# Kernel optimization log

Hardware: AMD Instinct MI355X
Metric: run time of the kernel (lower is better)

The kernel has to match this reference:

```python
import jax, jax.numpy as jnp
import numpy as np

DEPTH = 10          # floor(log2(nIn)) with nIn = 1024
N_NODES = 2 ** DEPTH - 1  # 1023
N_IN = 1024
N_OUT = 1024
N_BATCH = 65536


def _unit_rows(key, n, d):
    w = jax.random.normal(key, (n, d), dtype=jnp.float32)
    return w / jnp.linalg.norm(w, axis=-1, keepdims=True)


def setup_inputs() -> dict:
    key = jax.random.key(0)
    kx, kX, kY = jax.random.split(key, 3)
    x = jax.random.normal(kx, (N_BATCH, N_IN), dtype=jnp.float32)
    X = _unit_rows(kX, N_NODES, N_IN)   # hyperspherical-shell init
    Y = _unit_rows(kY, N_NODES, N_OUT)
    return {"x": x, "X": X, "Y": Y}


def reference(x, X, Y):
    # Fast-feedforward binary-tree routing: at each depth, every sample
    # dots with its current node's X row, accumulates lambda * Y row,
    # then branches left/right based on sign(lambda).
    n_batch = x.shape[0]
    n_out = Y.shape[-1]

    def step(carry, _):
        node, y = carry                            # node: [b] int32, y: [b, nOut]
        lam = jnp.einsum('bi,bi->b', x, X[node])   # gather + dot
        y = y + lam[:, None] * Y[node]             # gather + axpy
        node = node * 2 + 1 + (lam > 0).astype(node.dtype)
        return (node, y), None

    init = (jnp.zeros((n_batch,), dtype=jnp.int32),
            jnp.zeros((n_batch, n_out), dtype=x.dtype))
    (_, y), _ = jax.lax.scan(step, init, None, length=DEPTH)
    return y
```

## Files before the change

### kernel.cpp

```cpp
#include <hip/hip_runtime.h>


constexpr int DEPTH = 10;
constexpr int N_IN  = 1024;
constexpr int N_OUT = 1024;

__global__ __launch_bounds__(256) void fff_fwd(
        const float* __restrict__ xg,
        const float* __restrict__ Xg,
        const float* __restrict__ Yg,
        float* __restrict__ outg,
        int n_batch)
{
    const int lane = threadIdx.x & 63;
    const int wave = blockIdx.x * (blockDim.x >> 6) + (threadIdx.x >> 6);
    if (wave >= n_batch) return;

    const float4* xp = reinterpret_cast<const float4*>(xg + (size_t)wave * N_IN) + lane;
    float4 xv[4];
#pragma unroll
    for (int c = 0; c < 4; ++c) xv[c] = xp[c * 64];

    float4 acc[4];
#pragma unroll
    for (int c = 0; c < 4; ++c) acc[c] = make_float4(0.f, 0.f, 0.f, 0.f);

    int node = 0;
#pragma unroll
    for (int d = 0; d < DEPTH; ++d) {
        const float4* Xp = reinterpret_cast<const float4*>(Xg + (size_t)node * N_IN) + lane;
        const float4* Yp = reinterpret_cast<const float4*>(Yg + (size_t)node * N_IN) + lane;
        float4 xr[4], yr[4];
#pragma unroll
        for (int c = 0; c < 4; ++c) xr[c] = Xp[c * 64];
#pragma unroll
        for (int c = 0; c < 4; ++c) yr[c] = Yp[c * 64];

        double p = 0.0;
#pragma unroll
        for (int c = 0; c < 4; ++c) {
            p = fma((double)xv[c].x, (double)xr[c].x, p);
            p = fma((double)xv[c].y, (double)xr[c].y, p);
            p = fma((double)xv[c].z, (double)xr[c].z, p);
            p = fma((double)xv[c].w, (double)xr[c].w, p);
        }
#pragma unroll
        for (int off = 32; off > 0; off >>= 1)
            p += __shfl_xor(p, off, 64);

        const float lam = (float)p;

#pragma unroll
        for (int c = 0; c < 4; ++c) {
            acc[c].x = fmaf(lam, yr[c].x, acc[c].x);
            acc[c].y = fmaf(lam, yr[c].y, acc[c].y);
            acc[c].z = fmaf(lam, yr[c].z, acc[c].z);
            acc[c].w = fmaf(lam, yr[c].w, acc[c].w);
        }

        const int go_right = (p > 0.0) ? 1 : 0;
        node = __builtin_amdgcn_readfirstlane(node * 2 + 1 + go_right);
    }

    float4* op = reinterpret_cast<float4*>(outg + (size_t)wave * N_OUT) + lane;
#pragma unroll
    for (int c = 0; c < 4; ++c) op[c * 64] = acc[c];
}

extern "C" void kernel_launch(void* const* d_in, const int* in_sizes, int n_in,
                              void* d_out, int out_size, void* d_ws, size_t ws_size,
                              hipStream_t stream) {
    const float* x = (const float*)d_in[0];
    const float* X = (const float*)d_in[1];
    const float* Y = (const float*)d_in[2];
    float* out = (float*)d_out;

    const int n_batch = in_sizes[0] / N_IN;
    const int waves_per_block = 4;
    const int blocks = (n_batch + waves_per_block - 1) / waves_per_block;

    fff_fwd<<<blocks, 256, 0, stream>>>(x, X, Y, out, n_batch);
}
```

Before: 602.2 us.

## Speculatively compute both child dot products to break the tree-routing dependency chain

Each level now loads the X rows of both children and computes their partial dot products before the branch decision is known. The next level then only has to pick one, do the wave reduction and load Y. This hides gather latency behind the reduction and FMA work, and the partial sums are split into four accumulators to shorten the FP64 chain. The cost is roughly twice the X-row traffic and FP64 work, plus higher register pressure.

```diff
diff --git a/kernel.cpp b/kernel.cpp
--- a/kernel.cpp
+++ b/kernel.cpp
@@ -4,6 +4,45 @@
 constexpr int DEPTH = 10;
 constexpr int N_IN  = 1024;
 constexpr int N_OUT = 1024;
+
+__device__ __forceinline__ void load_row(float4 (&dst)[4],
+                                         const float* __restrict__ base,
+                                         int row, int lane)
+{
+    const float4* p = reinterpret_cast<const float4*>(base + (size_t)row * N_IN) + lane;
+#pragma unroll
+    for (int c = 0; c < 4; ++c) dst[c] = p[c * 64];
+}
+
+__device__ __forceinline__ double dot16(const float4 (&a)[4], const float4 (&b)[4])
+{
+    double p0 = 0.0, p1 = 0.0, p2 = 0.0, p3 = 0.0;
+    p0 = fma((double)a[0].x, (double)b[0].x, p0);
+    p0 = fma((double)a[0].y, (double)b[0].y, p0);
+    p0 = fma((double)a[0].z, (double)b[0].z, p0);
+    p0 = fma((double)a[0].w, (double)b[0].w, p0);
+    p1 = fma((double)a[1].x, (double)b[1].x, p1);
+    p1 = fma((double)a[1].y, (double)b[1].y, p1);
+    p1 = fma((double)a[1].z, (double)b[1].z, p1);
+    p1 = fma((double)a[1].w, (double)b[1].w, p1);
+    p2 = fma((double)a[2].x, (double)b[2].x, p2);
+    p2 = fma((double)a[2].y, (double)b[2].y, p2);
+    p2 = fma((double)a[2].z, (double)b[2].z, p2);
+    p2 = fma((double)a[2].w, (double)b[2].w, p2);
+    p3 = fma((double)a[3].x, (double)b[3].x, p3);
+    p3 = fma((double)a[3].y, (double)b[3].y, p3);
+    p3 = fma((double)a[3].z, (double)b[3].z, p3);
+    p3 = fma((double)a[3].w, (double)b[3].w, p3);
+    return (p0 + p1) + (p2 + p3);
+}
+
+__device__ __forceinline__ double wave_sum64(double p)
+{
+#pragma unroll
+    for (int off = 32; off > 0; off >>= 1)
+        p += __shfl_xor(p, off, 64);
+    return p;
+}
 
 __global__ __launch_bounds__(256) void fff_fwd(
         const float* __restrict__ xg,
@@ -25,41 +64,57 @@
 #pragma unroll
     for (int c = 0; c < 4; ++c) acc[c] = make_float4(0.f, 0.f, 0.f, 0.f);
 
-    int node = 0;
+    float4 cur[4], xl[4], xr[4], yv[4];
+    load_row(cur, Xg, 0, lane);
+    load_row(xl,  Xg, 1, lane);
+    load_row(xr,  Xg, 2, lane);
+    load_row(yv,  Yg, 0, lane);
+
+    double p = dot16(xv, cur);
+    p = wave_sum64(p);
+    int   s   = (p > 0.0) ? 1 : 0;
+    float lam = (float)p;
 #pragma unroll
-    for (int d = 0; d < DEPTH; ++d) {
-        const float4* Xp = reinterpret_cast<const float4*>(Xg + (size_t)node * N_IN) + lane;
-        const float4* Yp = reinterpret_cast<const float4*>(Yg + (size_t)node * N_IN) + lane;
-        float4 xr[4], yr[4];
+    for (int c = 0; c < 4; ++c) {
+        acc[c].x = fmaf(lam, yv[c].x, acc[c].x);
+        acc[c].y = fmaf(lam, yv[c].y, acc[c].y);
+        acc[c].z = fmaf(lam, yv[c].z, acc[c].z);
+        acc[c].w = fmaf(lam, yv[c].w, acc[c].w);
+    }
+
+    double pl = dot16(xv, xl);
+    double pr = dot16(xv, xr);
+
+    int node = __builtin_amdgcn_readfirstlane(1 + s);
+
 #pragma unroll
-        for (int c = 0; c < 4; ++c) xr[c] = Xp[c * 64];
-#pragma unroll
-        for (int c = 0; c < 4; ++c) yr[c] = Yp[c * 64];
+    for (int d = 1; d < DEPTH; ++d) {
+        if (d < DEPTH - 1) {
+            load_row(xl, Xg, 2 * node + 1, lane);
+            load_row(xr, Xg, 2 * node + 2, lane);
+        }
+        load_row(yv, Yg, node, lane);
 
-        double p = 0.0;
-#pragma unroll
-        for (int c = 0; c < 4; ++c) {
-            p = fma((double)xv[c].x, (double)xr[c].x, p);
-            p = fma((double)xv[c].y, (double)xr[c].y, p);
-            p = fma((double)xv[c].z, (double)xr[c].z, p);
-            p = fma((double)xv[c].w, (double)xr[c].w, p);
+        p = s ? pr : pl;
+        p = wave_sum64(p);
+        const int snew = (p > 0.0) ? 1 : 0;
+        lam = (float)p;
+
+        if (d < DEPTH - 1) {
+            pl = dot16(xv, xl);
+            pr = dot16(xv, xr);
         }
-#pragma unroll
-        for (int off = 32; off > 0; off >>= 1)
-            p += __shfl_xor(p, off, 64);
-
-        const float lam = (float)p;
 
 #pragma unroll
         for (int c = 0; c < 4; ++c) {
-            acc[c].x = fmaf(lam, yr[c].x, acc[c].x);
-            acc[c].y = fmaf(lam, yr[c].y, acc[c].y);
-            acc[c].z = fmaf(lam, yr[c].z, acc[c].z);
-            acc[c].w = fmaf(lam, yr[c].w, acc[c].w);
+            acc[c].x = fmaf(lam, yv[c].x, acc[c].x);
+            acc[c].y = fmaf(lam, yv[c].y, acc[c].y);
+            acc[c].z = fmaf(lam, yv[c].z, acc[c].z);
+            acc[c].w = fmaf(lam, yv[c].w, acc[c].w);
         }
 
-        const int go_right = (p > 0.0) ? 1 : 0;
-        node = __builtin_amdgcn_readfirstlane(node * 2 + 1 + go_right);
+        s = snew;
+        node = __builtin_amdgcn_readfirstlane(2 * node + 1 + snew);
     }
 
     float4* op = reinterpret_cast<float4*>(outg + (size_t)wave * N_OUT) + lane;
```

After: 685.4 us. 13.8% more time.

## Stage top four tree levels of X and Y in LDS per block

Applied to the files above, without the earlier changes.

Each 1024-thread block copies the first 15 nodes of X and Y (120 KB) into shared memory, then serves the first four tree depths from LDS instead of global memory. The block size grows from 256 to 1024 threads, and the double-precision dot product is split into four independent accumulators to shorten the FMA dependency chain. The per-block LDS fill adds startup cost and the large LDS footprint limits occupancy to about one block per CU. The four-accumulator summation can also change rounding slightly near the sign decision.

```diff
diff --git a/kernel.cpp b/kernel.cpp
--- a/kernel.cpp
+++ b/kernel.cpp
@@ -1,19 +1,76 @@
 #include <hip/hip_runtime.h>
 
 
-constexpr int DEPTH = 10;
-constexpr int N_IN  = 1024;
-constexpr int N_OUT = 1024;
+constexpr int DEPTH     = 10;
+constexpr int N_IN      = 1024;
+constexpr int N_OUT     = 1024;
+constexpr int LDS_DEPTHS = 4;
+constexpr int LDS_NODES  = 15;
+constexpr int THREADS    = 1024;
 
-__global__ __launch_bounds__(256) void fff_fwd(
+__device__ __forceinline__ void load_row4(float4 (&dst)[4], const float* __restrict__ row, int lane)
+{
+    const float4* p = reinterpret_cast<const float4*>(row) + lane;
+#pragma unroll
+    for (int c = 0; c < 4; ++c) dst[c] = p[c * 64];
+}
+
+__device__ __forceinline__ double dot16(const float4 (&a)[4], const float4 (&b)[4])
+{
+    double p0 = 0.0, p1 = 0.0, p2 = 0.0, p3 = 0.0;
+    p0 = fma((double)a[0].x, (double)b[0].x, p0);
+    p0 = fma((double)a[0].y, (double)b[0].y, p0);
+    p0 = fma((double)a[0].z, (double)b[0].z, p0);
+    p0 = fma((double)a[0].w, (double)b[0].w, p0);
+    p1 = fma((double)a[1].x, (double)b[1].x, p1);
+    p1 = fma((double)a[1].y, (double)b[1].y, p1);
+    p1 = fma((double)a[1].z, (double)b[1].z, p1);
+    p1 = fma((double)a[1].w, (double)b[1].w, p1);
+    p2 = fma((double)a[2].x, (double)b[2].x, p2);
+    p2 = fma((double)a[2].y, (double)b[2].y, p2);
+    p2 = fma((double)a[2].z, (double)b[2].z, p2);
+    p2 = fma((double)a[2].w, (double)b[2].w, p2);
+    p3 = fma((double)a[3].x, (double)b[3].x, p3);
+    p3 = fma((double)a[3].y, (double)b[3].y, p3);
+    p3 = fma((double)a[3].z, (double)b[3].z, p3);
+    p3 = fma((double)a[3].w, (double)b[3].w, p3);
+    return (p0 + p1) + (p2 + p3);
+}
+
+__device__ __forceinline__ double wave_sum64(double p)
+{
+#pragma unroll
+    for (int off = 32; off > 0; off >>= 1)
+        p += __shfl_xor(p, off, 64);
+    return p;
+}
+
+__global__ __launch_bounds__(THREADS) void fff_fwd(
         const float* __restrict__ xg,
         const float* __restrict__ Xg,
         const float* __restrict__ Yg,
         float* __restrict__ outg,
         int n_batch)
 {
+    extern __shared__ float lds[];
+    float* sX = lds;
+    float* sY = lds + LDS_NODES * N_IN;
+
+    {
+        const float4* gx4 = reinterpret_cast<const float4*>(Xg);
+        const float4* gy4 = reinterpret_cast<const float4*>(Yg);
+        float4* sx4 = reinterpret_cast<float4*>(sX);
+        float4* sy4 = reinterpret_cast<float4*>(sY);
+        const int n4 = LDS_NODES * N_IN / 4;
+        for (int i = threadIdx.x; i < n4; i += THREADS) {
+            sx4[i] = gx4[i];
+            sy4[i] = gy4[i];
+        }
+    }
+    __syncthreads();
+
     const int lane = threadIdx.x & 63;
-    const int wave = blockIdx.x * (blockDim.x >> 6) + (threadIdx.x >> 6);
+    const int wave = blockIdx.x * (THREADS >> 6) + (threadIdx.x >> 6);
     if (wave >= n_batch) return;
 
     const float4* xp = reinterpret_cast<const float4*>(xg + (size_t)wave * N_IN) + lane;
@@ -28,26 +85,17 @@
     int node = 0;
 #pragma unroll
     for (int d = 0; d < DEPTH; ++d) {
-        const float4* Xp = reinterpret_cast<const float4*>(Xg + (size_t)node * N_IN) + lane;
-        const float4* Yp = reinterpret_cast<const float4*>(Yg + (size_t)node * N_IN) + lane;
         float4 xr[4], yr[4];
-#pragma unroll
-        for (int c = 0; c < 4; ++c) xr[c] = Xp[c * 64];
-#pragma unroll
-        for (int c = 0; c < 4; ++c) yr[c] = Yp[c * 64];
+        if (d < LDS_DEPTHS) {
+            load_row4(xr, sX + node * N_IN, lane);
+            load_row4(yr, sY + node * N_IN, lane);
+        } else {
+            load_row4(xr, Xg + (size_t)node * N_IN, lane);
+            load_row4(yr, Yg + (size_t)node * N_IN, lane);
+        }
 
-        double p = 0.0;
-#pragma unroll
-        for (int c = 0; c < 4; ++c) {
-            p = fma((double)xv[c].x, (double)xr[c].x, p);
-            p = fma((double)xv[c].y, (double)xr[c].y, p);
-            p = fma((double)xv[c].z, (double)xr[c].z, p);
-            p = fma((double)xv[c].w, (double)xr[c].w, p);
-        }
-#pragma unroll
-        for (int off = 32; off > 0; off >>= 1)
-            p += __shfl_xor(p, off, 64);
-
+        double p = dot16(xv, xr);
+        p = wave_sum64(p);
         const float lam = (float)p;
 
 #pragma unroll
@@ -76,8 +124,16 @@
     float* out = (float*)d_out;
 
     const int n_batch = in_sizes[0] / N_IN;
-    const int waves_per_block = 4;
-    const int blocks = (n_batch + waves_per_block - 1) / waves_per_block;
+    const int blocks  = (n_batch + (THREADS >> 6) - 1) / (THREADS >> 6);
+    const size_t smem = (size_t)2 * LDS_NODES * N_IN * sizeof(float);
 
-    fff_fwd<<<blocks, 256, 0, stream>>>(x, X, Y, out, n_batch);
+    static bool attr_set = false;
+    if (!attr_set) {
+        (void)hipFuncSetAttribute((const void*)fff_fwd,
+                                  hipFuncAttributeMaxDynamicSharedMemorySize,
+                                  (int)smem);
+        attr_set = true;
+    }
+
+    fff_fwd<<<blocks, THREADS, smem, stream>>>(x, X, Y, out, n_batch);
 }
```

After: 569.4 us. -5.4%, faster.
